# Performance work log

Hardware: AMD Instinct MI355X
Metric: run time of the kernel (lower is better)

## Reference

```python
import jax, jax.numpy as jnp
import numpy as np

MAX_REL = 128  # max_relative_distance


def _rel_index(t_q, t_k, s):
    # relative_distances[i, j] = clip(i - j, -s, s) + min(s + 1, max(t_q, t_k)) - 1
    rd = jnp.arange(t_q)[:, None] - jnp.arange(t_k)[None, :]
    rd = jnp.clip(rd, -s, s)
    return rd + min(s + 1, max(t_q, t_k)) - 1  # (t_q, t_k), values in [0, 2s]


def setup_inputs() -> dict:
    key = jax.random.key(0)
    k1, k2, k3 = jax.random.split(key, 3)
    m, h, t, d = 4, 16, 1024, 128
    Q = jax.random.normal(k1, (m, h, t, d), dtype=jnp.float32)
    K = jax.random.normal(k2, (m, h, t, d), dtype=jnp.float32)
    pe = jax.random.normal(k3, (2 * MAX_REL + 1, d), dtype=jnp.float32)
    return {"Q": Q, "K": K, "pe": pe}


def reference(Q, K, pe):
    # Original: attn_rpes[t, d, s] = pe[idx[t, s], d]; out = einsum('mhtd,tds->mhts', Q, attn_rpes)
    # Equivalent (gather after matmul): out[m,h,t,s] = (Q @ pe^T)[m,h,t, idx[t,s]]
    t_q, t_k = Q.shape[2], K.shape[2]
    idx = _rel_index(t_q, t_k, MAX_REL)                     # (t_q, t_k) int32
    rel = jnp.einsum('mhtd,rd->mhtr', Q, pe)                # (m, h, t_q, 2s+1)
    out = jnp.take_along_axis(rel, idx[None, None, :, :], axis=-1)  # (m, h, t_q, t_k)
    return out
```

## Files before the change

kernel.cpp:

```cpp
#include <hip/hip_runtime.h>

constexpr int D_DIM = 128;
constexpr int T_Q   = 1024;
constexpr int NPE   = 257;
constexpr int WAVES = 16;
constexpr int BLOCK_THREADS  = WAVES * 64;
constexpr int ROWS_PER_BLOCK = 256;

typedef __attribute__((ext_vector_type(8))) short short8;
typedef __attribute__((ext_vector_type(4))) float f32x4;

#define RL(V, SRC) __uint_as_float(__builtin_amdgcn_readlane(__float_as_uint(V), (SRC)))

__global__ __launch_bounds__(BLOCK_THREADS, 4)
void rpe_mfma(const float* __restrict__ Q,
              const float* __restrict__ pe,
              float* __restrict__ out)
{
    __shared__ ushort phi[NPE * 128];
    __shared__ float  rev[WAVES][4][264];

    const int tid = threadIdx.x;
    const int w   = tid >> 6;
    const int l   = tid & 63;
    const int n15 = l & 15;
    const int g   = l >> 4;

    for (int q4 = tid; q4 < NPE * 32; q4 += BLOCK_THREADS) {
        const int n  = q4 >> 5;
        const int d0 = (q4 & 31) * 4;
        const float4 f = *reinterpret_cast<const float4*>(pe + n * 128 + d0);
        const float fv[4] = {f.x, f.y, f.z, f.w};
        ushort h[4];
#pragma unroll
        for (int e = 0; e < 4; ++e) {
            const uint u = __float_as_uint(fv[e]);
            h[e] = (ushort)((u + 0x7FFFu + ((u >> 16) & 1u)) >> 16);
        }
        const int posr0 = (d0 + 8 * (n & 15)) & 127;
        *reinterpret_cast<uint2*>(&phi[n * 128 + posr0]) = *reinterpret_cast<uint2*>(h);
    }
    __syncthreads();

    const int waveRow0 = blockIdx.x * ROWS_PER_BLOCK + w * 16;

    const float* qrow = Q + (size_t)(waveRow0 + n15) * D_DIM;
    short8 ahi[4], alo[4];
#pragma unroll
    for (int kk = 0; kk < 4; ++kk) {
        const int base = 32 * kk + 8 * g;
        const float4 a0 = *reinterpret_cast<const float4*>(qrow + base);
        const float4 a1 = *reinterpret_cast<const float4*>(qrow + base + 4);
        const float av[8] = {a0.x, a0.y, a0.z, a0.w, a1.x, a1.y, a1.z, a1.w};
#pragma unroll
        for (int e = 0; e < 8; ++e) {
            const uint u = __float_as_uint(av[e]);
            ahi[kk][e] = (short)(u >> 16);
            const float fl = av[e] - __uint_as_float(u & 0xffff0000u);
            alo[kk][e] = (short)(__float_as_uint(fl) >> 16);
        }
    }

    f32x4 acc[16];
#pragma unroll
    for (int j = 0; j < 16; ++j) acc[j] = (f32x4){0.f, 0.f, 0.f, 0.f};

#pragma unroll
    for (int kk = 0; kk < 4; ++kk) {
        const int posr = ((32 * kk + 8 * g) + 8 * n15) & 127;
#pragma unroll
        for (int j = 0; j < 16; ++j) {
            const short8 bh = *reinterpret_cast<const short8*>(&phi[(16 * j + n15) * 128 + posr]);
            acc[j] = __builtin_amdgcn_mfma_f32_16x16x32_bf16(ahi[kk], bh, acc[j], 0, 0, 0);
            acc[j] = __builtin_amdgcn_mfma_f32_16x16x32_bf16(alo[kk], bh, acc[j], 0, 0, 0);
        }
    }

    float rel_part = 0.f;
#pragma unroll
    for (int kk = 0; kk < 4; ++kk) {
        const short8 ph = *reinterpret_cast<const short8*>(&phi[256 * 128 + 32 * kk + 8 * g]);
#pragma unroll
        for (int e = 0; e < 8; ++e) {
            const float qv = __uint_as_float(((uint)(ushort)ahi[kk][e]) << 16)
                           + __uint_as_float(((uint)(ushort)alo[kk][e]) << 16);
            const float pv = __uint_as_float(((uint)(ushort)ph[e]) << 16);
            rel_part = fmaf(qv, pv, rel_part);
        }
    }
    rel_part += __shfl_xor(rel_part, 16, 64);
    rel_part += __shfl_xor(rel_part, 32, 64);

#pragma unroll
    for (int c = 0; c < 4; ++c) {
#pragma unroll
        for (int j = 0; j < 16; ++j)
            rev[w][g][256 + c - 16 * j - n15] = acc[j][c];

        {
            const float rel_r = __shfl(rel_part, 4 * g + c, 64);
            const float r0_r  = __shfl(acc[0][c], 16 * g, 64);
            if (n15 <= 3) {
                if (n15 <= c) rev[w][g][n15] = rel_r;
            } else if (n15 <= 10) {
                const int p = 253 + n15;
                if (p >= 257 + c) rev[w][g][p] = r0_r;
            }
        }

#pragma unroll
        for (int u = 0; u < 4; ++u) {
            const int gRow = waveRow0 + 4 * u + c;
            const int t = gRow & (T_Q - 1);
            const int ofs = 128 - t + c;
            float* orow = out + (size_t)gRow * T_Q;
            const float rr256 = RL(rel_part, 4 * u + c);
            const float rr0   = RL(acc[0][c], 16 * u);

#pragma unroll
            for (int k = 0; k < 4; ++k) {
                const int s0 = 4 * l + 256 * k;
                const int j0 = t + 128 - s0;
                float4 v;
                if (j0 <= 0) {
                    v = make_float4(rr0, rr0, rr0, rr0);
                } else if (j0 >= 259) {
                    v = make_float4(rr256, rr256, rr256, rr256);
                } else {
                    v = *reinterpret_cast<const float4*>(&rev[w][u][s0 + ofs]);
                }
                reinterpret_cast<float4*>(orow)[l + 64 * k] = v;
            }
        }
    }
}

extern "C" void kernel_launch(void* const* d_in, const int* in_sizes, int n_in,
                              void* d_out, int out_size, void* d_ws, size_t ws_size,
                              hipStream_t stream)
{
    const float* Q  = (const float*)d_in[0];
    const float* pe = (const float*)d_in[2];
    float* out = (float*)d_out;

    const int total_rows = in_sizes[0] / D_DIM;
    const int grid = total_rows / ROWS_PER_BLOCK;
    rpe_mfma<<<grid, BLOCK_THREADS, 0, stream>>>(Q, pe, out);
}
```

Before: 75.74 us.

## Shrink blocks to four waves, stage results in bf16, use nontemporal stores

```diff
diff --git a/kernel.cpp b/kernel.cpp
--- a/kernel.cpp
+++ b/kernel.cpp
@@ -2,23 +2,27 @@
 
 constexpr int D_DIM = 128;
 constexpr int T_Q   = 1024;
-constexpr int NPE   = 257;
-constexpr int WAVES = 16;
+constexpr int WAVES = 4;
 constexpr int BLOCK_THREADS  = WAVES * 64;
-constexpr int ROWS_PER_BLOCK = 256;
+constexpr int ROWS_PER_BLOCK = 64;
 
 typedef __attribute__((ext_vector_type(8))) short short8;
 typedef __attribute__((ext_vector_type(4))) float f32x4;
 
 #define RL(V, SRC) __uint_as_float(__builtin_amdgcn_readlane(__float_as_uint(V), (SRC)))
 
-__global__ __launch_bounds__(BLOCK_THREADS, 4)
+__device__ __forceinline__ ushort f32_to_bf16_rne(float f) {
+    const uint u = __float_as_uint(f);
+    return (ushort)((u + 0x7FFFu + ((u >> 16) & 1u)) >> 16);
+}
+
+__global__ __launch_bounds__(BLOCK_THREADS, 2)
 void rpe_mfma(const float* __restrict__ Q,
               const float* __restrict__ pe,
               float* __restrict__ out)
 {
-    __shared__ ushort phi[NPE * 128];
-    __shared__ float  rev[WAVES][4][264];
+    __shared__ ushort phi[256 * 128];
+    __shared__ ushort rev[WAVES][4][264];
 
     const int tid = threadIdx.x;
     const int w   = tid >> 6;
@@ -26,17 +30,12 @@
     const int n15 = l & 15;
     const int g   = l >> 4;
 
-    for (int q4 = tid; q4 < NPE * 32; q4 += BLOCK_THREADS) {
+    for (int q4 = tid; q4 < 256 * 32; q4 += BLOCK_THREADS) {
         const int n  = q4 >> 5;
         const int d0 = (q4 & 31) * 4;
         const float4 f = *reinterpret_cast<const float4*>(pe + n * 128 + d0);
-        const float fv[4] = {f.x, f.y, f.z, f.w};
-        ushort h[4];
-#pragma unroll
-        for (int e = 0; e < 4; ++e) {
-            const uint u = __float_as_uint(fv[e]);
-            h[e] = (ushort)((u + 0x7FFFu + ((u >> 16) & 1u)) >> 16);
-        }
+        ushort h[4] = { f32_to_bf16_rne(f.x), f32_to_bf16_rne(f.y),
+                        f32_to_bf16_rne(f.z), f32_to_bf16_rne(f.w) };
         const int posr0 = (d0 + 8 * (n & 15)) & 127;
         *reinterpret_cast<uint2*>(&phi[n * 128 + posr0]) = *reinterpret_cast<uint2*>(h);
     }
@@ -79,13 +78,15 @@
     float rel_part = 0.f;
 #pragma unroll
     for (int kk = 0; kk < 4; ++kk) {
-        const short8 ph = *reinterpret_cast<const short8*>(&phi[256 * 128 + 32 * kk + 8 * g]);
+        const float* p256 = pe + 256 * 128 + 32 * kk + 8 * g;
+        const float4 pA = *reinterpret_cast<const float4*>(p256);
+        const float4 pB = *reinterpret_cast<const float4*>(p256 + 4);
+        const float pv[8] = {pA.x, pA.y, pA.z, pA.w, pB.x, pB.y, pB.z, pB.w};
 #pragma unroll
         for (int e = 0; e < 8; ++e) {
             const float qv = __uint_as_float(((uint)(ushort)ahi[kk][e]) << 16)
                            + __uint_as_float(((uint)(ushort)alo[kk][e]) << 16);
-            const float pv = __uint_as_float(((uint)(ushort)ph[e]) << 16);
-            rel_part = fmaf(qv, pv, rel_part);
+            rel_part = fmaf(qv, pv[e], rel_part);
         }
     }
     rel_part += __shfl_xor(rel_part, 16, 64);
@@ -95,16 +96,16 @@
     for (int c = 0; c < 4; ++c) {
 #pragma unroll
         for (int j = 0; j < 16; ++j)
-            rev[w][g][256 + c - 16 * j - n15] = acc[j][c];
+            rev[w][g][256 + c - 16 * j - n15] = f32_to_bf16_rne(acc[j][c]);
 
         {
             const float rel_r = __shfl(rel_part, 4 * g + c, 64);
             const float r0_r  = __shfl(acc[0][c], 16 * g, 64);
             if (n15 <= 3) {
-                if (n15 <= c) rev[w][g][n15] = rel_r;
+                if (n15 <= c) rev[w][g][n15] = f32_to_bf16_rne(rel_r);
             } else if (n15 <= 10) {
                 const int p = 253 + n15;
-                if (p >= 257 + c) rev[w][g][p] = r0_r;
+                if (p >= 257 + c) rev[w][g][p] = f32_to_bf16_rne(r0_r);
             }
         }
 
@@ -121,15 +122,19 @@
             for (int k = 0; k < 4; ++k) {
                 const int s0 = 4 * l + 256 * k;
                 const int j0 = t + 128 - s0;
-                float4 v;
+                f32x4 v;
                 if (j0 <= 0) {
-                    v = make_float4(rr0, rr0, rr0, rr0);
+                    v = (f32x4){rr0, rr0, rr0, rr0};
                 } else if (j0 >= 259) {
-                    v = make_float4(rr256, rr256, rr256, rr256);
+                    v = (f32x4){rr256, rr256, rr256, rr256};
                 } else {
-                    v = *reinterpret_cast<const float4*>(&rev[w][u][s0 + ofs]);
+                    const uint2 rr = *reinterpret_cast<const uint2*>(&rev[w][u][s0 + ofs]);
+                    v = (f32x4){ __uint_as_float(rr.x << 16),
+                                 __uint_as_float(rr.x & 0xffff0000u),
+                                 __uint_as_float(rr.y << 16),
+                                 __uint_as_float(rr.y & 0xffff0000u) };
                 }
-                reinterpret_cast<float4*>(orow)[l + 64 * k] = v;
+                __builtin_nontemporal_store(v, reinterpret_cast<f32x4*>(orow) + (l + 64 * k));
             }
         }
     }
```

Measured after the change: 66.02 us. -12.8%, faster.
